# Kernel optimization log

Measured on AMD Instinct MI355X. Metric: run time of the kernel, lower is better.

The kernel has to match this reference:

```python
import jax, jax.numpy as jnp
import numpy as np

NBINS = 256


def _getmask(mi):
    # mi: [h, w] image already scaled to [0, 255]
    # torch.histc(mi, bins=256, min=0, max=255): values outside [0,255] ignored
    hist = jax.lax.stop_gradient(
        jnp.histogram(mi, bins=NBINS, range=(0.0, 255.0))[0].astype(jnp.float32)
    )
    # mask_output[i] = sum_j |j - i| * hist[j]  -> small 256x256 matvec
    j = jnp.arange(NBINS, dtype=jnp.float32)
    dist = jnp.abs(j[:, None] - j[None, :])  # [256, 256]
    mask_output = dist @ hist                 # [256]
    # mask[image==i] = mask_output[i]; only exact-integer pixels in [0,255] match
    r = jnp.round(mi)
    valid = (mi == r) & (r >= 0.0) & (r <= 255.0)
    idx = jnp.clip(r, 0.0, 255.0).astype(jnp.int32)
    mask = jnp.where(valid, mask_output[idx], 0.0)
    # if mask.max()==0: return zeros; else return the (scaled) image itself
    return jnp.where(mask.max() == 0.0, jnp.zeros_like(mi), mi)


def _forward(image_irr, image_vis):
    irr = image_irr * 255.0
    _vis = image_vis * 255.0  # computed but unused in the original forward
    mi = irr[:, 0, :, :]                       # [b, h, w]
    masked = jax.vmap(_getmask)(mi) / 255.0    # [b, h, w]
    msk_ir = masked[:, None, :, :]             # [b, 1, h, w]
    msk = jnp.stack([msk_ir, 1.0 - msk_ir], axis=0)  # [2, b, 1, h, w]
    msks = jax.nn.softmax(msk, axis=0)
    return msks[0], msks[1]


def setup_inputs() -> dict:
    key = jax.random.key(0)
    k1, k2 = jax.random.split(key)
    shape = (16, 1, 1024, 1024)
    # quantized pixels so that image*255 is (mostly) exactly integer,
    # matching the module's implicit assumption (histc + equality tests)
    image_irr = jax.random.randint(k1, shape, 0, 256).astype(jnp.float32) / 255.0
    image_vis = jax.random.randint(k2, shape, 0, 256).astype(jnp.float32) / 255.0
    return {"image_irr": image_irr, "image_vis": image_vis}


def reference(image_irr, image_vis):
    return _forward(image_irr, image_vis)
```

## Files before the change

### kernel.cpp

```cpp
#include <hip/hip_runtime.h>
#include <stdint.h>

#define BATCH 16
#define HW (1024*1024)
#define NPIX (BATCH * HW)
#define SBLK 64

typedef float vf4 __attribute__((ext_vector_type(4)));

__global__ __launch_bounds__(256) void scan_kernel(const float* __restrict__ in,
                                                   uint2* __restrict__ partials) {
    const int tid = threadIdx.x;
    const int batch = blockIdx.y;
    int minb = 0x7FFF, maxb = -1, valid = 0;

    const vf4* src = (const vf4*)(in + (size_t)batch * HW) + (size_t)blockIdx.x * 4096;
    for (int i = tid; i < 4096; i += 256) {
        vf4 x = src[i];
        float v[4] = {x.x, x.y, x.z, x.w};
#pragma unroll
        for (int k = 0; k < 4; ++k) {
            float mi = v[k] * 255.0f;
            if (mi >= 0.0f && mi <= 255.0f) {
                int b = (int)(mi * (256.0f / 255.0f));
                if (b > 255) b = 255;
                minb = min(minb, b);
                maxb = max(maxb, b);
                valid |= (mi == rintf(mi)) ? 1 : 0;
            }
        }
    }
#pragma unroll
    for (int off = 32; off > 0; off >>= 1) {
        minb  = min(minb, __shfl_xor(minb, off));
        maxb  = max(maxb, __shfl_xor(maxb, off));
        valid |= __shfl_xor(valid, off);
    }
    __shared__ int sm[4], sx[4], sv[4];
    const int w = tid >> 6;
    if ((tid & 63) == 0) { sm[w] = minb; sx[w] = maxb; sv[w] = valid; }
    __syncthreads();
    if (tid == 0) {
#pragma unroll
        for (int i = 1; i < 4; ++i) {
            minb  = min(minb, sm[i]);
            maxb  = max(maxb, sx[i]);
            valid |= sv[i];
        }
        uint2 p;
        p.x = ((unsigned)(minb & 0xFFFF) << 16) | (unsigned)(maxb & 0xFFFF);
        p.y = (unsigned)valid;
        partials[batch * SBLK + blockIdx.x] = p;
    }
}

__device__ __forceinline__ float2 softmax2(float x, float fm) {
    float mi = x * 255.0f;
    float m = (mi / 255.0f) * fm;
    float e = expf(1.0f - 2.0f * m);
    float r = 1.0f / (1.0f + e);
    return make_float2(r, e * r);
}

__global__ __launch_bounds__(256) void out_kernel(const float* __restrict__ in,
                                                  const uint2* __restrict__ partials,
                                                  float* __restrict__ out) {
    const int batch = blockIdx.x >> 10;
    const size_t i4 = (size_t)blockIdx.x * 256 + threadIdx.x;

    vf4 x = ((const vf4*)in)[i4];

    __shared__ float s_fm;
    if (threadIdx.x < 64) {
        uint2 p = partials[batch * SBLK + threadIdx.x];
        int minb = (int)(short)(p.x >> 16);
        int maxb = (int)(short)(p.x & 0xFFFF);
        unsigned valid = p.y;
#pragma unroll
        for (int off = 32; off > 0; off >>= 1) {
            minb = min(minb, __shfl_xor(minb, off));
            maxb = max(maxb, __shfl_xor(maxb, off));
            valid |= (unsigned)__shfl_xor((int)valid, off);
        }
        if (threadIdx.x == 0) s_fm = (valid && (minb != maxb)) ? 1.0f : 0.0f;
    }
    __syncthreads();
    const float fm = s_fm;

    float2 rx = softmax2(x.x, fm);
    float2 ry = softmax2(x.y, fm);
    float2 rz = softmax2(x.z, fm);
    float2 rw = softmax2(x.w, fm);
    vf4 o0 = {rx.x, ry.x, rz.x, rw.x};
    vf4 o1 = {rx.y, ry.y, rz.y, rw.y};
    __builtin_nontemporal_store(o0, &((vf4*)out)[i4]);
    __builtin_nontemporal_store(o1, &((vf4*)(out + (size_t)NPIX))[i4]);
}

extern "C" void kernel_launch(void* const* d_in, const int* in_sizes, int n_in,
                              void* d_out, int out_size, void* d_ws, size_t ws_size,
                              hipStream_t stream) {
    const float* irr = (const float*)d_in[0];
    float* out = (float*)d_out;

    uint2* partials = (uint2*)d_ws;

    scan_kernel<<<dim3(SBLK, BATCH), 256, 0, stream>>>(irr, partials);
    out_kernel<<<NPIX / 4 / 256, 256, 0, stream>>>(irr, partials, out);
}
```

Measured before the change: 224.8 us.

## Fuse scan and softmax into one kernel with per-batch atomic flag handoff

Replaces the separate scan and output kernels with one persistent-style kernel. Each block holds its 16 vec4 loads in registers, publishes partial min/max/valid, and the last block per batch (tracked by an atomic counter) computes the flag that the other blocks spin-wait on. The aim is to read the input only once instead of twice and to drop a kernel launch. The cost is a memset, inter-block spin waits that assume all 1024 blocks can be co-resident, and higher register pressure.

```diff
diff --git a/kernel.cpp b/kernel.cpp
--- a/kernel.cpp
+++ b/kernel.cpp
@@ -4,20 +4,42 @@
 #define BATCH 16
 #define HW (1024*1024)
 #define NPIX (BATCH * HW)
-#define SBLK 64
+#define GRID 1024
+#define TPB 256
+#define VPT 16
+#define V4B (TPB * VPT)
+#define BPB (GRID / BATCH)
 
 typedef float vf4 __attribute__((ext_vector_type(4)));
 
-__global__ __launch_bounds__(256) void scan_kernel(const float* __restrict__ in,
-                                                   uint2* __restrict__ partials) {
+__device__ __forceinline__ float2 softmax2(float x, float fm) {
+    float mi = x * 255.0f;
+    float m = (mi / 255.0f) * fm;
+    float e = expf(1.0f - 2.0f * m);
+    float r = 1.0f / (1.0f + e);
+    return make_float2(r, e * r);
+}
+
+__global__ __launch_bounds__(TPB, 4) void fused_kernel(const float* __restrict__ in,
+                                                       unsigned* __restrict__ ctr,
+                                                       unsigned* __restrict__ flagw,
+                                                       unsigned long long* __restrict__ partials,
+                                                       float* __restrict__ out) {
     const int tid = threadIdx.x;
-    const int batch = blockIdx.y;
+    const int blk = blockIdx.x;
+    const int batch = blk >> 6;
+    const size_t base = (size_t)blk * V4B + tid;
+
+    const vf4* src = (const vf4*)in;
+    vf4 d[VPT];
+#pragma unroll
+    for (int j = 0; j < VPT; ++j)
+        d[j] = __builtin_nontemporal_load(&src[base + (size_t)j * TPB]);
+
     int minb = 0x7FFF, maxb = -1, valid = 0;
-
-    const vf4* src = (const vf4*)(in + (size_t)batch * HW) + (size_t)blockIdx.x * 4096;
-    for (int i = tid; i < 4096; i += 256) {
-        vf4 x = src[i];
-        float v[4] = {x.x, x.y, x.z, x.w};
+#pragma unroll
+    for (int j = 0; j < VPT; ++j) {
+        float v[4] = {d[j].x, d[j].y, d[j].z, d[j].w};
 #pragma unroll
         for (int k = 0; k < 4; ++k) {
             float mi = v[k] * 255.0f;
@@ -37,6 +59,8 @@
         valid |= __shfl_xor(valid, off);
     }
     __shared__ int sm[4], sx[4], sv[4];
+    __shared__ unsigned s_last;
+    __shared__ float s_fm;
     const int w = tid >> 6;
     if ((tid & 63) == 0) { sm[w] = minb; sx[w] = maxb; sv[w] = valid; }
     __syncthreads();
@@ -47,54 +71,62 @@
             maxb  = max(maxb, sx[i]);
             valid |= sv[i];
         }
-        uint2 p;
-        p.x = ((unsigned)(minb & 0xFFFF) << 16) | (unsigned)(maxb & 0xFFFF);
-        p.y = (unsigned)valid;
-        partials[batch * SBLK + blockIdx.x] = p;
+        unsigned long long p =
+            ((unsigned long long)(unsigned)(((minb & 0xFFFF) << 16) | (maxb & 0xFFFF)) << 32)
+            | (unsigned)valid;
+        __hip_atomic_store(&partials[blk], p, __ATOMIC_RELAXED, __HIP_MEMORY_SCOPE_AGENT);
+        unsigned old = __hip_atomic_fetch_add(&ctr[batch], 1u,
+                                              __ATOMIC_ACQ_REL, __HIP_MEMORY_SCOPE_AGENT);
+        s_last = (old == BPB - 1) ? 1u : 0u;
     }
-}
+    __syncthreads();
 
-__device__ __forceinline__ float2 softmax2(float x, float fm) {
-    float mi = x * 255.0f;
-    float m = (mi / 255.0f) * fm;
-    float e = expf(1.0f - 2.0f * m);
-    float r = 1.0f / (1.0f + e);
-    return make_float2(r, e * r);
-}
-
-__global__ __launch_bounds__(256) void out_kernel(const float* __restrict__ in,
-                                                  const uint2* __restrict__ partials,
-                                                  float* __restrict__ out) {
-    const int batch = blockIdx.x >> 10;
-    const size_t i4 = (size_t)blockIdx.x * 256 + threadIdx.x;
-
-    vf4 x = ((const vf4*)in)[i4];
-
-    __shared__ float s_fm;
-    if (threadIdx.x < 64) {
-        uint2 p = partials[batch * SBLK + threadIdx.x];
-        int minb = (int)(short)(p.x >> 16);
-        int maxb = (int)(short)(p.x & 0xFFFF);
-        unsigned valid = p.y;
+    if (s_last) {
+        if (tid < 64) {
+            unsigned long long p = __hip_atomic_load(&partials[batch * BPB + tid],
+                                                     __ATOMIC_RELAXED, __HIP_MEMORY_SCOPE_AGENT);
+            int mn = (int)(short)(p >> 48);
+            int mx = (int)(short)(p >> 32);
+            unsigned vv = (unsigned)p;
 #pragma unroll
-        for (int off = 32; off > 0; off >>= 1) {
-            minb = min(minb, __shfl_xor(minb, off));
-            maxb = max(maxb, __shfl_xor(maxb, off));
-            valid |= (unsigned)__shfl_xor((int)valid, off);
+            for (int off = 32; off > 0; off >>= 1) {
+                mn = min(mn, __shfl_xor(mn, off));
+                mx = max(mx, __shfl_xor(mx, off));
+                vv |= (unsigned)__shfl_xor((int)vv, off);
+            }
+            if (tid == 0) {
+                unsigned f = (vv && (mn != mx)) ? 3u : 2u;
+                __hip_atomic_store(&flagw[batch], f,
+                                   __ATOMIC_RELAXED, __HIP_MEMORY_SCOPE_SYSTEM);
+                s_fm = (float)(f & 1u);
+            }
         }
-        if (threadIdx.x == 0) s_fm = (valid && (minb != maxb)) ? 1.0f : 0.0f;
+    } else if (tid == 0) {
+        unsigned f;
+        for (;;) {
+            f = __hip_atomic_load(&flagw[batch], __ATOMIC_RELAXED, __HIP_MEMORY_SCOPE_SYSTEM);
+            if (f) break;
+            __builtin_amdgcn_s_sleep(2);
+        }
+        s_fm = (float)(f & 1u);
     }
     __syncthreads();
     const float fm = s_fm;
 
-    float2 rx = softmax2(x.x, fm);
-    float2 ry = softmax2(x.y, fm);
-    float2 rz = softmax2(x.z, fm);
-    float2 rw = softmax2(x.w, fm);
-    vf4 o0 = {rx.x, ry.x, rz.x, rw.x};
-    vf4 o1 = {rx.y, ry.y, rz.y, rw.y};
-    __builtin_nontemporal_store(o0, &((vf4*)out)[i4]);
-    __builtin_nontemporal_store(o1, &((vf4*)(out + (size_t)NPIX))[i4]);
+    vf4* o0p = (vf4*)out;
+    vf4* o1p = (vf4*)(out + (size_t)NPIX);
+#pragma unroll
+    for (int j = 0; j < VPT; ++j) {
+        float2 rx = softmax2(d[j].x, fm);
+        float2 ry = softmax2(d[j].y, fm);
+        float2 rz = softmax2(d[j].z, fm);
+        float2 rw = softmax2(d[j].w, fm);
+        vf4 o0 = {rx.x, ry.x, rz.x, rw.x};
+        vf4 o1 = {rx.y, ry.y, rz.y, rw.y};
+        const size_t idx = base + (size_t)j * TPB;
+        __builtin_nontemporal_store(o0, &o0p[idx]);
+        __builtin_nontemporal_store(o1, &o1p[idx]);
+    }
 }
 
 extern "C" void kernel_launch(void* const* d_in, const int* in_sizes, int n_in,
@@ -103,8 +135,11 @@
     const float* irr = (const float*)d_in[0];
     float* out = (float*)d_out;
 
-    uint2* partials = (uint2*)d_ws;
+    unsigned* ctr   = (unsigned*)d_ws;
+    unsigned* flagw = ctr + 16;
+    unsigned long long* partials = (unsigned long long*)((char*)d_ws + 256);
 
-    scan_kernel<<<dim3(SBLK, BATCH), 256, 0, stream>>>(irr, partials);
-    out_kernel<<<NPIX / 4 / 256, 256, 0, stream>>>(irr, partials, out);
+    hipMemsetAsync(d_ws, 0, 128, stream);
+
+    fused_kernel<<<GRID, TPB, 0, stream>>>(irr, ctr, flagw, partials, out);
 }
```

Measured after the change: 298.2 us. 1.33x slower.

## Early-exit scan via per-batch proof flag and widen output blocks

Applied to the files above, without the earlier changes.

The scan kernel first checks a small 256-vector slice per block. If that slice already shows a valid pixel and distinct bins, it sets a per-batch proof flag in global memory, and other blocks poll the flag periodically to skip the rest of their scan. The output kernel now processes eight vec4s per thread with fewer blocks and reads the proof flag when deciding the mask. A memset of the flag buffer is added per launch, and the early exit depends on data that usually satisfies the condition quickly.

```diff
diff --git a/kernel.cpp b/kernel.cpp
--- a/kernel.cpp
+++ b/kernel.cpp
@@ -4,53 +4,105 @@
 #define BATCH 16
 #define HW (1024*1024)
 #define NPIX (BATCH * HW)
+#define NV4 (NPIX / 4)
 #define SBLK 64
+#define SGRID (SBLK * BATCH)
+#define SV4 4096
+#define OGRID 2048
+#define OVPT 8
+#define OV4B (256 * OVPT)
 
 typedef float vf4 __attribute__((ext_vector_type(4)));
 
-__global__ __launch_bounds__(256) void scan_kernel(const float* __restrict__ in,
-                                                   uint2* __restrict__ partials) {
-    const int tid = threadIdx.x;
-    const int batch = blockIdx.y;
-    int minb = 0x7FFF, maxb = -1, valid = 0;
 
-    const vf4* src = (const vf4*)(in + (size_t)batch * HW) + (size_t)blockIdx.x * 4096;
-    for (int i = tid; i < 4096; i += 256) {
-        vf4 x = src[i];
-        float v[4] = {x.x, x.y, x.z, x.w};
+__device__ __forceinline__ void accum4(vf4 x, int& minb, int& maxb, int& valid) {
+    float v[4] = {x.x, x.y, x.z, x.w};
 #pragma unroll
-        for (int k = 0; k < 4; ++k) {
-            float mi = v[k] * 255.0f;
-            if (mi >= 0.0f && mi <= 255.0f) {
-                int b = (int)(mi * (256.0f / 255.0f));
-                if (b > 255) b = 255;
-                minb = min(minb, b);
-                maxb = max(maxb, b);
-                valid |= (mi == rintf(mi)) ? 1 : 0;
-            }
+    for (int k = 0; k < 4; ++k) {
+        float mi = v[k] * 255.0f;
+        if (mi >= 0.0f && mi <= 255.0f) {
+            int b = (int)(mi * (256.0f / 255.0f));
+            if (b > 255) b = 255;
+            minb = min(minb, b);
+            maxb = max(maxb, b);
+            valid |= (mi == rintf(mi)) ? 1 : 0;
         }
     }
+}
+
+__device__ __forceinline__ void wave_reduce(int& minb, int& maxb, int& valid) {
 #pragma unroll
     for (int off = 32; off > 0; off >>= 1) {
         minb  = min(minb, __shfl_xor(minb, off));
         maxb  = max(maxb, __shfl_xor(maxb, off));
         valid |= __shfl_xor(valid, off);
     }
+}
+
+__global__ __launch_bounds__(256) void scan_kernel(const float* __restrict__ in,
+                                                   unsigned* __restrict__ proofs,
+                                                   uint2* __restrict__ partials) {
+    const int tid = threadIdx.x;
+    const int blk = blockIdx.x;
+    const int batch = blk >> 6;
+    const vf4* src = (const vf4*)in + (size_t)blk * SV4;
+
     __shared__ int sm[4], sx[4], sv[4];
+    __shared__ int s_proof;
     const int w = tid >> 6;
+
+    int minb = 0x7FFF, maxb = -1, valid = 0;
+    accum4(src[tid], minb, maxb, valid);
+    wave_reduce(minb, maxb, valid);
     if ((tid & 63) == 0) { sm[w] = minb; sx[w] = maxb; sv[w] = valid; }
     __syncthreads();
     if (tid == 0) {
+        int mn = sm[0], mx = sx[0], vv = sv[0];
 #pragma unroll
-        for (int i = 1; i < 4; ++i) {
-            minb  = min(minb, sm[i]);
-            maxb  = max(maxb, sx[i]);
-            valid |= sv[i];
+        for (int i = 1; i < 4; ++i) { mn = min(mn, sm[i]); mx = max(mx, sx[i]); vv |= sv[i]; }
+        if (vv && mn != mx) {
+            __hip_atomic_store(&proofs[batch], 1u, __ATOMIC_RELAXED, __HIP_MEMORY_SCOPE_AGENT);
+            s_proof = 1;
+        } else {
+            s_proof = (int)__hip_atomic_load(&proofs[batch], __ATOMIC_RELAXED, __HIP_MEMORY_SCOPE_AGENT);
         }
-        uint2 p;
-        p.x = ((unsigned)(minb & 0xFFFF) << 16) | (unsigned)(maxb & 0xFFFF);
-        p.y = (unsigned)valid;
-        partials[batch * SBLK + blockIdx.x] = p;
+    }
+    __syncthreads();
+    int skip = s_proof;
+
+    if (!skip) {
+        minb = 0x7FFF; maxb = -1; valid = 0;
+        for (int j = 0; j < 16; ++j) {
+            if (j == 4 || j == 8 || j == 12) {
+                __syncthreads();
+                if (tid == 0)
+                    s_proof = (int)__hip_atomic_load(&proofs[batch], __ATOMIC_RELAXED,
+                                                     __HIP_MEMORY_SCOPE_AGENT);
+                __syncthreads();
+                if (s_proof) { skip = 1; break; }
+            }
+            accum4(src[tid + j * 256], minb, maxb, valid);
+        }
+        if (!skip) {
+            wave_reduce(minb, maxb, valid);
+            if ((tid & 63) == 0) { sm[w] = minb; sx[w] = maxb; sv[w] = valid; }
+            __syncthreads();
+            if (tid == 0) {
+#pragma unroll
+                for (int i = 1; i < 4; ++i) {
+                    minb  = min(minb, sm[i]);
+                    maxb  = max(maxb, sx[i]);
+                    valid |= sv[i];
+                }
+                uint2 p;
+                p.x = ((unsigned)(minb & 0xFFFF) << 16) | (unsigned)(maxb & 0xFFFF);
+                p.y = (unsigned)valid;
+                partials[blk] = p;
+            }
+        }
+    }
+    if (skip && tid == 0) {
+        partials[blk] = make_uint2(0x7FFFFFFFu, 0u);
     }
 }
 
@@ -63,38 +115,54 @@
 }
 
 __global__ __launch_bounds__(256) void out_kernel(const float* __restrict__ in,
+                                                  const unsigned* __restrict__ proofs,
                                                   const uint2* __restrict__ partials,
                                                   float* __restrict__ out) {
-    const int batch = blockIdx.x >> 10;
-    const size_t i4 = (size_t)blockIdx.x * 256 + threadIdx.x;
+    const int tid = threadIdx.x;
+    const int blk = blockIdx.x;
+    const int batch = blk >> 7;
+    const size_t base = (size_t)blk * OV4B + tid;
 
-    vf4 x = ((const vf4*)in)[i4];
+    const vf4* src = (const vf4*)in;
+    vf4 d[OVPT];
+#pragma unroll
+    for (int j = 0; j < OVPT; ++j)
+        d[j] = src[base + (size_t)j * 256];
 
     __shared__ float s_fm;
-    if (threadIdx.x < 64) {
-        uint2 p = partials[batch * SBLK + threadIdx.x];
-        int minb = (int)(short)(p.x >> 16);
-        int maxb = (int)(short)(p.x & 0xFFFF);
-        unsigned valid = p.y;
+    if (tid < 64) {
+        uint2 p = partials[batch * SBLK + tid];
+        int mn = (int)(short)(p.x >> 16);
+        int mx = (int)(short)(p.x & 0xFFFF);
+        unsigned vv = p.y;
 #pragma unroll
         for (int off = 32; off > 0; off >>= 1) {
-            minb = min(minb, __shfl_xor(minb, off));
-            maxb = max(maxb, __shfl_xor(maxb, off));
-            valid |= (unsigned)__shfl_xor((int)valid, off);
+            mn = min(mn, __shfl_xor(mn, off));
+            mx = max(mx, __shfl_xor(mx, off));
+            vv |= (unsigned)__shfl_xor((int)vv, off);
         }
-        if (threadIdx.x == 0) s_fm = (valid && (minb != maxb)) ? 1.0f : 0.0f;
+        if (tid == 0) {
+            unsigned pr = proofs[batch];
+            s_fm = (pr || (vv && mn != mx)) ? 1.0f : 0.0f;
+        }
     }
     __syncthreads();
     const float fm = s_fm;
 
-    float2 rx = softmax2(x.x, fm);
-    float2 ry = softmax2(x.y, fm);
-    float2 rz = softmax2(x.z, fm);
-    float2 rw = softmax2(x.w, fm);
-    vf4 o0 = {rx.x, ry.x, rz.x, rw.x};
-    vf4 o1 = {rx.y, ry.y, rz.y, rw.y};
-    __builtin_nontemporal_store(o0, &((vf4*)out)[i4]);
-    __builtin_nontemporal_store(o1, &((vf4*)(out + (size_t)NPIX))[i4]);
+    vf4* o0p = (vf4*)out;
+    vf4* o1p = (vf4*)(out + (size_t)NPIX);
+#pragma unroll
+    for (int j = 0; j < OVPT; ++j) {
+        float2 rx = softmax2(d[j].x, fm);
+        float2 ry = softmax2(d[j].y, fm);
+        float2 rz = softmax2(d[j].z, fm);
+        float2 rw = softmax2(d[j].w, fm);
+        vf4 o0 = {rx.x, ry.x, rz.x, rw.x};
+        vf4 o1 = {rx.y, ry.y, rz.y, rw.y};
+        const size_t idx = base + (size_t)j * 256;
+        __builtin_nontemporal_store(o0, &o0p[idx]);
+        __builtin_nontemporal_store(o1, &o1p[idx]);
+    }
 }
 
 extern "C" void kernel_launch(void* const* d_in, const int* in_sizes, int n_in,
@@ -103,8 +171,11 @@
     const float* irr = (const float*)d_in[0];
     float* out = (float*)d_out;
 
-    uint2* partials = (uint2*)d_ws;
+    unsigned* proofs = (unsigned*)d_ws;
+    uint2* partials  = (uint2*)((char*)d_ws + 256);
 
-    scan_kernel<<<dim3(SBLK, BATCH), 256, 0, stream>>>(irr, partials);
-    out_kernel<<<NPIX / 4 / 256, 256, 0, stream>>>(irr, partials, out);
+    hipMemsetAsync(d_ws, 0, 64, stream);
+
+    scan_kernel<<<SGRID, 256, 0, stream>>>(irr, proofs, partials);
+    out_kernel<<<OGRID, 256, 0, stream>>>(irr, proofs, partials, out);
 }
```

New measurement: 258.4 us. +15.0%, slower.
